# Performance work log

Measured on AMD Instinct MI355X. Metric: run time of the kernel, lower is better.

## Reference

```python
import jax, jax.numpy as jnp
import numpy as np

D_INPUT = 2048
DD_DIM = 512
DD_PAIRS = DD_DIM // 2


def setup_inputs() -> dict:
    key = jax.random.key(0)
    k1, k2, k3 = jax.random.split(key, 3)
    x = jax.random.normal(k1, (4, 4096, D_INPUT), dtype=jnp.float32)
    # Learned projection (zeros at init in torch; use small random for a non-trivial test)
    W = jax.random.normal(k2, (DD_PAIRS, D_INPUT), dtype=jnp.float32) * 0.02
    b = jax.random.normal(k3, (DD_PAIRS,), dtype=jnp.float32) * 0.02
    return {"x": x, "W": W, "b": b}


def reference(x, W, b):
    # x: (B, T, D); W: (P, D); b: (P,) with P = DD_DIM // 2
    deltas = jnp.einsum('btd,pd->btp', x, W) + b          # (B, T, P)
    angles = jnp.cumsum(deltas, axis=1)                   # cumulative phase
    cos, sin = jnp.cos(angles), jnp.sin(angles)
    x1 = x[..., :DD_PAIRS]                                # (B, T, P)
    x2 = x[..., DD_PAIRS:DD_DIM]                          # (B, T, P)
    rotated = jnp.concatenate([x1 * cos - x2 * sin, x2 * cos + x1 * sin], axis=-1)
    return jnp.concatenate([rotated, x[..., DD_DIM:]], axis=-1)
```

## Files before the change

### kernel.cpp

```cpp
#include <hip/hip_runtime.h>
#include <math.h>

#define BB 4
#define TT 4096
#define DDIM 2048
#define PP 256
#define MM (BB*TT)
#define KKDIM 2048
#define CHUNK 32
#define NCHUNK (TT/CHUNK)

#define BK 32
#define KSTEPS (KKDIM/BK)
#define LROW 72

typedef __attribute__((ext_vector_type(8))) short short8;
typedef __attribute__((ext_vector_type(4))) float f32x4;

__device__ __forceinline__ unsigned short f2bf(float f) {
    unsigned u = __float_as_uint(f);
    u += 0x7FFF + ((u >> 16) & 1);
    return (unsigned short)(u >> 16);
}
__device__ __forceinline__ float bf2f(unsigned short h) {
    return __uint_as_float(((unsigned)h) << 16);
}

__device__ __forceinline__ void cvt8(const float4& va, const float4& vb,
                                     short8& hi, short8& lo) {
    float f[8] = {va.x, va.y, va.z, va.w, vb.x, vb.y, vb.z, vb.w};
    #pragma unroll
    for (int j = 0; j < 8; ++j) {
        unsigned short h = f2bf(f[j]);
        hi[j] = (short)h;
        lo[j] = (short)f2bf(f[j] - bf2f(h));
    }
}

__device__ __forceinline__ void cvt4(const float4& v, uint2& hp, uint2& lp) {
    unsigned short h0 = f2bf(v.x), h1 = f2bf(v.y), h2 = f2bf(v.z), h3 = f2bf(v.w);
    unsigned short l0 = f2bf(v.x - bf2f(h0)), l1 = f2bf(v.y - bf2f(h1));
    unsigned short l2 = f2bf(v.z - bf2f(h2)), l3 = f2bf(v.w - bf2f(h3));
    hp.x = (unsigned)h0 | ((unsigned)h1 << 16); hp.y = (unsigned)h2 | ((unsigned)h3 << 16);
    lp.x = (unsigned)l0 | ((unsigned)l1 << 16); lp.y = (unsigned)l2 | ((unsigned)l3 << 16);
}

__global__ __launch_bounds__(256) void prep_wf_k(const float* __restrict__ W,
                                                 unsigned short* __restrict__ Wfh,
                                                 unsigned short* __restrict__ Wfl) {
    const int f = blockIdx.x * 256 + threadIdx.x;
    const int lane = f & 63;
    const int nb   = (f >> 6) & 15;
    const int k0i  = f >> 10;
    const int row  = nb * 16 + (lane & 15);
    const int kk   = k0i * 32 + (lane >> 4) * 8;
    const float* src = W + (size_t)row * KKDIM + kk;
    float4 a = *(const float4*)src;
    float4 b = *(const float4*)(src + 4);
    short8 hi, lo;
    cvt8(a, b, hi, lo);
    *(short8*)(Wfh + (size_t)f * 8) = hi;
    *(short8*)(Wfl + (size_t)f * 8) = lo;
}

#define GBAR()                                                                 \
    do {                                                                       \
        asm volatile("s_waitcnt lgkmcnt(0)" ::: "memory");                     \
        __builtin_amdgcn_sched_barrier(0);                                     \
        __builtin_amdgcn_s_barrier();                                          \
        __builtin_amdgcn_sched_barrier(0);                                     \
    } while (0)

#define GSTEP(CUR, NXT, BHc, BLc, BHn, BLn, ANa0, ANa1, AFa0, AFa1, IT)        \
{                                                                              \
    const int itN_ = (IT) + 1;                                                 \
    const int itF_ = ((IT) + 2 < KSTEPS) ? (IT) + 2 : KSTEPS - 1;              \
                \
    AFa0 = *(const float4*)(xs0 + itF_ * BK);                                  \
    AFa1 = *(const float4*)(xs1 + itF_ * BK);                                  \
                                              \
    const int k0iN_ = (itN_ < KSTEPS) ? itN_ : KSTEPS - 1;                     \
    _Pragma("unroll")                                                          \
    for (int nt = 0; nt < 2; ++nt) {                                           \
        size_t o = bfbase + (size_t)(k0iN_ * 16 + nt) * 512;                   \
        BHn[nt] = *(const short8*)(Wfh + o);                                   \
        BLn[nt] = *(const short8*)(Wfl + o);                                   \
    }                                                                          \
       \
    {                                                                          \
        uint2 hp_, lp_;                                                        \
        cvt4(ANa0, hp_, lp_);                                                  \
        *(uint2*)&Ast[NXT][sidx0]      = hp_;                                  \
        *(uint2*)&Ast[NXT][sidx0 + 32] = lp_;                                  \
        cvt4(ANa1, hp_, lp_);                                                  \
        *(uint2*)&Ast[NXT][sidx1]      = hp_;                                  \
        *(uint2*)&Ast[NXT][sidx1 + 32] = lp_;                                  \
    }                                                                          \
                                    \
    if (docopy && itN_ < KSTEPS) {                                             \
        const int kN_ = itN_ * BK;                                             \
        if (kN_ >= 512) {                                                      \
            *(float4*)(os0 + kN_) = ANa0;                                      \
            *(float4*)(os1 + kN_) = ANa1;                                      \
        }                                                                      \
    }                                                                          \
                                     \
    short8 ah_[2], al_[2];                                                     \
    _Pragma("unroll")                                                          \
    for (int mt = 0; mt < 2; ++mt) {                                           \
        int idx = (wm * 32 + mt * 16 + lm) * LROW + ko * 8;                    \
        ah_[mt] = *(const short8*)&Ast[CUR][idx];                              \
        al_[mt] = *(const short8*)&Ast[CUR][idx + 32];                         \
    }                                                                          \
    _Pragma("unroll")                                                          \
    for (int mt = 0; mt < 2; ++mt)                                             \
        _Pragma("unroll")                                                      \
        for (int nt = 0; nt < 2; ++nt) {                                       \
            f32x4 c = acc[mt][nt];                                             \
            c = __builtin_amdgcn_mfma_f32_16x16x32_bf16(ah_[mt], BHc[nt], c, 0, 0, 0); \
            c = __builtin_amdgcn_mfma_f32_16x16x32_bf16(ah_[mt], BLc[nt], c, 0, 0, 0); \
            c = __builtin_amdgcn_mfma_f32_16x16x32_bf16(al_[mt], BHc[nt], c, 0, 0, 0); \
            acc[mt][nt] = c;                                                   \
        }                                                                      \
    GBAR();                                                                    \
}

__global__ __launch_bounds__(512, 4) void gemm5_k(const float* __restrict__ x,
                                                  const unsigned short* __restrict__ Wfh,
                                                  const unsigned short* __restrict__ Wfl,
                                                  const float* __restrict__ bias,
                                                  float* __restrict__ delta,
                                                  float* __restrict__ csum,
                                                  float* __restrict__ out) {
    __shared__ unsigned short Ast[2][128 * LROW];

    const int hw      = blockIdx.y * 4 + blockIdx.x;
    const int logical = (hw & 7) * 64 + (hw >> 3);
    const int nidx    = logical & 3;
    const int midx    = logical >> 2;
    const int n0      = nidx * 64;
    const int m0      = midx * 128;
    const bool docopy = (nidx == 0);

    const int tid  = threadIdx.x;
    const int w    = tid >> 6;
    const int wm   = w >> 1;
    const int wn   = w & 1;
    const int lane = tid & 63;
    const int lm   = lane & 15;
    const int ko   = lane >> 4;

    const int arow0 = tid >> 3;
    const int ach   = tid & 7;
    const int sidx0 = arow0 * LROW + ach * 4;
    const int sidx1 = (64 + arow0) * LROW + ach * 4;
    const float* xs0 = x + (size_t)(m0 + arow0) * KKDIM + ach * 4;
    const float* xs1 = x + (size_t)(m0 + 64 + arow0) * KKDIM + ach * 4;
    float* os0 = out + (size_t)(m0 + arow0) * DDIM + ach * 4;
    float* os1 = out + (size_t)(m0 + 64 + arow0) * DDIM + ach * 4;

    const size_t bfbase = ((size_t)(nidx * 4 + wn * 2) * 64 + (size_t)lane) * 8;

    f32x4 acc[2][2];
    #pragma unroll
    for (int i = 0; i < 2; ++i)
        #pragma unroll
        for (int j = 0; j < 2; ++j) {
            f32x4 z = {0.f, 0.f, 0.f, 0.f};
            acc[i][j] = z;
        }

    float4 aA0, aA1, aB0, aB1;
    short8 bhA[2], blA[2], bhB[2], blB[2];

    {
        float4 p0 = *(const float4*)(xs0);
        float4 p1 = *(const float4*)(xs1);
        aA0 = *(const float4*)(xs0 + BK);
        aA1 = *(const float4*)(xs1 + BK);
        #pragma unroll
        for (int nt = 0; nt < 2; ++nt) {
            size_t o = bfbase + (size_t)nt * 512;
            bhA[nt] = *(const short8*)(Wfh + o);
            blA[nt] = *(const short8*)(Wfl + o);
        }
        uint2 hp, lp;
        cvt4(p0, hp, lp);
        *(uint2*)&Ast[0][sidx0]      = hp;
        *(uint2*)&Ast[0][sidx0 + 32] = lp;
        cvt4(p1, hp, lp);
        *(uint2*)&Ast[0][sidx1]      = hp;
        *(uint2*)&Ast[0][sidx1 + 32] = lp;
        GBAR();
    }

    for (int it = 0; it < KSTEPS; it += 2) {
        GSTEP(0, 1, bhA, blA, bhB, blB, aA0, aA1, aB0, aB1, it)
        GSTEP(1, 0, bhB, blB, bhA, blA, aB0, aB1, aA0, aA1, it + 1)
    }

    float bsv[2];
    #pragma unroll
    for (int nt = 0; nt < 2; ++nt) bsv[nt] = bias[n0 + wn * 32 + nt * 16 + lm];

    float cs[2] = {0.f, 0.f};
    #pragma unroll
    for (int mt = 0; mt < 2; ++mt)
        #pragma unroll
        for (int nt = 0; nt < 2; ++nt)
            #pragma unroll
            for (int r = 0; r < 4; ++r) {
                float val = acc[mt][nt][r] + bsv[nt];
                int m = m0 + wm * 32 + mt * 16 + ko * 4 + r;
                delta[(size_t)m * PP + n0 + wn * 32 + nt * 16 + lm] = val;
                cs[nt] += val;
            }
    #pragma unroll
    for (int nt = 0; nt < 2; ++nt) {
        float s = cs[nt];
        s += __shfl_xor(s, 16);
        s += __shfl_xor(s, 32);
        if (lane < 16)
            csum[(size_t)(m0 / CHUNK + wm) * PP + n0 + wn * 32 + nt * 16 + lane] = s;
    }
}

__global__ __launch_bounds__(256) void rotate4_k(const float* __restrict__ delta,
                                                 const float* __restrict__ csum,
                                                 const float* __restrict__ x,
                                                 float* __restrict__ out) {
    const int blk = blockIdx.x;
    const int seg = blk & 3;
    const int bc  = blk >> 2;
    const int c   = bc & (NCHUNK - 1);
    const int b   = bc >> 7;
    const int p   = threadIdx.x;

    const float* cs = csum + (size_t)(b * NCHUNK) * PP + p;
    float angle = 0.f;
    int c0 = 0;
    for (; c0 + 16 <= c; c0 += 16) {
        float v[16];
        #pragma unroll
        for (int j = 0; j < 16; ++j) v[j] = cs[(size_t)(c0 + j) * PP];
        #pragma unroll
        for (int j = 0; j < 16; ++j) angle += v[j];
    }
    for (; c0 < c; ++c0) angle += cs[(size_t)c0 * PP];

    const int tbase = bc * CHUNK;
    const float* dp = delta + (size_t)tbase * PP + p;

    const int tpre = seg * 8;
    for (int t = 0; t < tpre; t += 8) {
        float v[8];
        #pragma unroll
        for (int j = 0; j < 8; ++j) v[j] = dp[(size_t)(t + j) * PP];
        #pragma unroll
        for (int j = 0; j < 8; ++j) angle += v[j];
    }

    const float* xp = x + (size_t)tbase * DDIM + p;
    float*       op = out + (size_t)tbase * DDIM + p;
    const float inv2pi = 0.15915494309189535f;

    for (int t0 = tpre; t0 < tpre + 8; t0 += 4) {
        float dv[4], x1v[4], x2v[4];
        #pragma unroll
        for (int j = 0; j < 4; ++j) {
            dv[j]  = dp[(size_t)(t0 + j) * PP];
            x1v[j] = xp[(size_t)(t0 + j) * DDIM];
            x2v[j] = xp[(size_t)(t0 + j) * DDIM + PP];
        }
        #pragma unroll
        for (int j = 0; j < 4; ++j) {
            angle += dv[j];
            float r  = __builtin_amdgcn_fractf(angle * inv2pi);
            float s  = __builtin_amdgcn_sinf(r);
            float co = __builtin_amdgcn_cosf(r);
            op[(size_t)(t0 + j) * DDIM]      = x1v[j] * co - x2v[j] * s;
            op[(size_t)(t0 + j) * DDIM + PP] = x2v[j] * co + x1v[j] * s;
        }
    }
}

__global__ __launch_bounds__(256) void gemm_k(const float* __restrict__ x,
                                              const float* __restrict__ W,
                                              const float* __restrict__ bias,
                                              float* __restrict__ delta,
                                              int dstride, int doff) {
    __shared__ float As[16][68];
    __shared__ float Bs[16][68];
    const int m0  = blockIdx.x * 64;
    const int n0  = blockIdx.y * 64;
    const int tid = threadIdx.x;
    const int lr  = tid >> 2;
    const int lc  = (tid & 3) << 2;
    const int tmi = tid & 15;
    const int tni = tid >> 4;
    float acc[4][4] = {};
    for (int k0 = 0; k0 < KKDIM; k0 += 16) {
        float4 a4 = *(const float4*)(x + (size_t)(m0 + lr) * KKDIM + k0 + lc);
        float4 b4 = *(const float4*)(W + (size_t)(n0 + lr) * KKDIM + k0 + lc);
        __syncthreads();
        As[lc + 0][lr] = a4.x; As[lc + 1][lr] = a4.y;
        As[lc + 2][lr] = a4.z; As[lc + 3][lr] = a4.w;
        Bs[lc + 0][lr] = b4.x; Bs[lc + 1][lr] = b4.y;
        Bs[lc + 2][lr] = b4.z; Bs[lc + 3][lr] = b4.w;
        __syncthreads();
        #pragma unroll
        for (int kk = 0; kk < 16; ++kk) {
            float4 av = *(const float4*)&As[kk][tmi * 4];
            float4 bv = *(const float4*)&Bs[kk][tni * 4];
            float am[4] = {av.x, av.y, av.z, av.w};
            float bn[4] = {bv.x, bv.y, bv.z, bv.w};
            #pragma unroll
            for (int i = 0; i < 4; ++i)
                #pragma unroll
                for (int j = 0; j < 4; ++j)
                    acc[i][j] += am[i] * bn[j];
        }
    }
    const float4 b4 = *(const float4*)(bias + n0 + tni * 4);
    #pragma unroll
    for (int i = 0; i < 4; ++i) {
        size_t m = (size_t)(m0 + tmi * 4 + i);
        float4 o;
        o.x = acc[i][0] + b4.x; o.y = acc[i][1] + b4.y;
        o.z = acc[i][2] + b4.z; o.w = acc[i][3] + b4.w;
        *(float4*)(delta + m * dstride + doff + n0 + tni * 4) = o;
    }
}

__global__ __launch_bounds__(256) void chunksum_k(const float* __restrict__ delta,
                                                  int dstride, int doff,
                                                  float* __restrict__ csum, int cstride) {
    const int bc = blockIdx.x;
    const int b  = bc / NCHUNK;
    const int c  = bc % NCHUNK;
    const int p  = threadIdx.x;
    const int tbase = b * TT + c * CHUNK;
    float s = 0.f;
    #pragma unroll 8
    for (int t = 0; t < CHUNK; ++t)
        s += delta[(size_t)(tbase + t) * dstride + doff + p];
    csum[(size_t)bc * cstride + p] = s;
}

__global__ __launch_bounds__(256) void scan_k(float* __restrict__ csum, int cstride) {
    const int idx = blockIdx.x * 256 + threadIdx.x;
    const int b = idx >> 8;
    const int p = idx & 255;
    float run = 0.f;
    for (int c0 = 0; c0 < NCHUNK; c0 += 8) {
        float v[8];
        #pragma unroll
        for (int j = 0; j < 8; ++j)
            v[j] = csum[(size_t)(b * NCHUNK + c0 + j) * cstride + p];
        #pragma unroll
        for (int j = 0; j < 8; ++j) {
            float t = v[j];
            csum[(size_t)(b * NCHUNK + c0 + j) * cstride + p] = run;
            run += t;
        }
    }
}

__global__ __launch_bounds__(256) void rotate_k(const float* __restrict__ delta,
                                                int dstride, int doff,
                                                const float* __restrict__ csum, int cstride,
                                                const float* __restrict__ x,
                                                float* __restrict__ out) {
    const int bc = blockIdx.x;
    const int p  = threadIdx.x;
    const int tbase = bc * CHUNK;
    float angle = csum[(size_t)bc * cstride + p];
    for (int t = 0; t < CHUNK; ++t) {
        size_t row = (size_t)(tbase + t);
        angle += delta[row * dstride + doff + p];
        float s, co;
        sincosf(angle, &s, &co);
        float x1 = x[row * DDIM + p];
        float x2 = x[row * DDIM + PP + p];
        out[row * DDIM + p]      = x1 * co - x2 * s;
        out[row * DDIM + PP + p] = x2 * co + x1 * s;
    }
}

__global__ __launch_bounds__(256) void copy_k(const float* __restrict__ x,
                                              float* __restrict__ out) {
    const size_t row = (size_t)blockIdx.x * 4 + (threadIdx.x >> 6);
    const int lane = threadIdx.x & 63;
    const int col = 512 + (blockIdx.y * 64 + lane) * 4;
    const size_t a = row * DDIM + col;
    *(float4*)(out + a) = *(const float4*)(x + a);
}

extern "C" void kernel_launch(void* const* d_in, const int* in_sizes, int n_in,
                              void* d_out, int out_size, void* d_ws, size_t ws_size,
                              hipStream_t stream) {
    const float* x    = (const float*)d_in[0];
    const float* W    = (const float*)d_in[1];
    const float* bias = (const float*)d_in[2];
    float* out = (float*)d_out;

    const size_t delta_elems = (size_t)MM * PP;
    const size_t csum_elems  = (size_t)BB * NCHUNK * PP;
    const size_t w_elems     = (size_t)PP * KKDIM;
    const size_t need = (delta_elems + csum_elems) * sizeof(float)
                      + 2 * w_elems * sizeof(unsigned short);

    if (ws_size >= need) {
        float* delta = (float*)d_ws;
        float* csum  = (float*)d_ws + delta_elems;
        unsigned short* Wfh = (unsigned short*)(csum + csum_elems);
        unsigned short* Wfl = Wfh + w_elems;
        prep_wf_k<<<256, 256, 0, stream>>>(W, Wfh, Wfl);
        gemm5_k<<<dim3(4, MM / 128), 512, 0, stream>>>(x, Wfh, Wfl, bias,
                                                       delta, csum, out);
        rotate4_k<<<BB * NCHUNK * 4, 256, 0, stream>>>(delta, csum, x, out);
    } else {
        float* delta = out; const int dstride = DDIM, doff = 512;
        float* csum  = out + 768; const int cstride = DDIM;
        gemm_k<<<dim3(MM / 64, PP / 64), 256, 0, stream>>>(x, W, bias, delta, dstride, doff);
        chunksum_k<<<BB * NCHUNK, 256, 0, stream>>>(delta, dstride, doff, csum, cstride);
        scan_k<<<(BB * PP) / 256, 256, 0, stream>>>(csum, cstride);
        rotate_k<<<BB * NCHUNK, 256, 0, stream>>>(delta, dstride, doff, csum, cstride, x, out);
        copy_k<<<dim3(MM / 4, 6), 256, 0, stream>>>(x, out);
    }
}
```

Baseline: 325.5 us.

## Restructure GEMM so each wave stages its own A rows and drop block barriers

The GEMM kernel moves from 512 threads with a 4x2 wave grid and a shared A tile to 256 threads where each wave owns 32 rows and stages its own private, XOR-swizzled LDS slice. Because no wave reads another wave's data, the per-k-step block barrier is removed. Each wave now covers a 32x64 tile (twice the N width), doubling B register fragments per step. The aim is to cut barrier stalls and LDS bank conflicts. In exchange, each wave loads the full B tile itself, so global and L2 traffic for W doubles, register pressure rises, and launch bounds drop to 2 blocks per CU.

Result: slower. 352.2 us (+8.2%).

```diff
diff --git a/kernel.cpp b/kernel.cpp
--- a/kernel.cpp
+++ b/kernel.cpp
@@ -12,7 +12,7 @@
 
 #define BK 32
 #define KSTEPS (KKDIM/BK)
-#define LROW 72
+#define LSLICE (32*128)
 
 typedef __attribute__((ext_vector_type(8))) short short8;
 typedef __attribute__((ext_vector_type(4))) float f32x4;
@@ -43,6 +43,10 @@
     unsigned short l2 = f2bf(v.z - bf2f(h2)), l3 = f2bf(v.w - bf2f(h3));
     hp.x = (unsigned)h0 | ((unsigned)h1 << 16); hp.y = (unsigned)h2 | ((unsigned)h3 << 16);
     lp.x = (unsigned)l0 | ((unsigned)l1 << 16); lp.y = (unsigned)l2 | ((unsigned)l3 << 16);
+}
+
+__device__ __forceinline__ int aoff(int row, int inner) {
+    return row * 128 + (inner ^ ((row & 7) << 4));
 }
 
 __global__ __launch_bounds__(256) void prep_wf_k(const float* __restrict__ W,
@@ -63,76 +67,68 @@
     *(short8*)(Wfl + (size_t)f * 8) = lo;
 }
 
-#define GBAR()                                                                 \
-    do {                                                                       \
-        asm volatile("s_waitcnt lgkmcnt(0)" ::: "memory");                     \
-        __builtin_amdgcn_sched_barrier(0);                                     \
-        __builtin_amdgcn_s_barrier();                                          \
-        __builtin_amdgcn_sched_barrier(0);                                     \
-    } while (0)
-
-#define GSTEP(CUR, NXT, BHc, BLc, BHn, BLn, ANa0, ANa1, AFa0, AFa1, IT)        \
+__device__ __forceinline__ void stageA(const float4 a[4], unsigned char* sb,
+                                       int r_, int q_) {
+    uint2 hp[4], lp[4];
+    #pragma unroll
+    for (int j = 0; j < 4; ++j) cvt4(a[j], hp[j], lp[j]);
+    uint4 h01 = {hp[0].x, hp[0].y, hp[1].x, hp[1].y};
+    uint4 h23 = {hp[2].x, hp[2].y, hp[3].x, hp[3].y};
+    uint4 l01 = {lp[0].x, lp[0].y, lp[1].x, lp[1].y};
+    uint4 l23 = {lp[2].x, lp[2].y, lp[3].x, lp[3].y};
+    *(uint4*)(sb + aoff(r_, q_ * 32))           = h01;
+    *(uint4*)(sb + aoff(r_, q_ * 32 + 16))      = h23;
+    *(uint4*)(sb + aoff(r_, 64 + q_ * 32))      = l01;
+    *(uint4*)(sb + aoff(r_, 64 + q_ * 32 + 16)) = l23;
+}
+
+#define GSTEP6(CUR, NXT, AC, AP, BC, BN, IT)                                   \
 {                                                                              \
-    const int itN_ = (IT) + 1;                                                 \
-    const int itF_ = ((IT) + 2 < KSTEPS) ? (IT) + 2 : KSTEPS - 1;              \
-                \
-    AFa0 = *(const float4*)(xs0 + itF_ * BK);                                  \
-    AFa1 = *(const float4*)(xs1 + itF_ * BK);                                  \
-                                              \
-    const int k0iN_ = (itN_ < KSTEPS) ? itN_ : KSTEPS - 1;                     \
+    const int itA_ = ((IT) + 2 < KSTEPS) ? (IT) + 2 : KSTEPS - 1;              \
+    const int itB_ = ((IT) + 1 < KSTEPS) ? (IT) + 1 : KSTEPS - 1;              \
     _Pragma("unroll")                                                          \
-    for (int nt = 0; nt < 2; ++nt) {                                           \
-        size_t o = bfbase + (size_t)(k0iN_ * 16 + nt) * 512;                   \
-        BHn[nt] = *(const short8*)(Wfh + o);                                   \
-        BLn[nt] = *(const short8*)(Wfl + o);                                   \
+    for (int j = 0; j < 4; ++j)                                                \
+        AP[j] = *(const float4*)(xsrc + (size_t)itA_ * BK + j * 4);            \
+    _Pragma("unroll")                                                          \
+    for (int nt = 0; nt < 4; ++nt) {                                           \
+        size_t o = bfbase + (size_t)itB_ * 8192 + (size_t)nt * 512;            \
+        BN[2 * nt]     = *(const short8*)(Wfh + o);                            \
+        BN[2 * nt + 1] = *(const short8*)(Wfl + o);                            \
     }                                                                          \
-       \
-    {                                                                          \
-        uint2 hp_, lp_;                                                        \
-        cvt4(ANa0, hp_, lp_);                                                  \
-        *(uint2*)&Ast[NXT][sidx0]      = hp_;                                  \
-        *(uint2*)&Ast[NXT][sidx0 + 32] = lp_;                                  \
-        cvt4(ANa1, hp_, lp_);                                                  \
-        *(uint2*)&Ast[NXT][sidx1]      = hp_;                                  \
-        *(uint2*)&Ast[NXT][sidx1 + 32] = lp_;                                  \
+    stageA(AC, sbW + (NXT) * LSLICE, r_, q_);         \
+    if (docopy && (IT) + 1 < KSTEPS && ((IT) + 1) * BK >= 512) {               \
+        _Pragma("unroll")                                                      \
+        for (int j = 0; j < 4; ++j)                                            \
+            *(float4*)(osrc + (size_t)((IT) + 1) * BK + j * 4) = AC[j];        \
     }                                                                          \
-                                    \
-    if (docopy && itN_ < KSTEPS) {                                             \
-        const int kN_ = itN_ * BK;                                             \
-        if (kN_ >= 512) {                                                      \
-            *(float4*)(os0 + kN_) = ANa0;                                      \
-            *(float4*)(os1 + kN_) = ANa1;                                      \
-        }                                                                      \
-    }                                                                          \
-                                     \
     short8 ah_[2], al_[2];                                                     \
     _Pragma("unroll")                                                          \
     for (int mt = 0; mt < 2; ++mt) {                                           \
-        int idx = (wm * 32 + mt * 16 + lm) * LROW + ko * 8;                    \
-        ah_[mt] = *(const short8*)&Ast[CUR][idx];                              \
-        al_[mt] = *(const short8*)&Ast[CUR][idx + 32];                         \
+        const unsigned char* sr = sbW + (CUR) * LSLICE;                        \
+        int row = mt * 16 + lm;                                                \
+        ah_[mt] = *(const short8*)(sr + aoff(row, ko * 16));                   \
+        al_[mt] = *(const short8*)(sr + aoff(row, 64 + ko * 16));              \
     }                                                                          \
     _Pragma("unroll")                                                          \
     for (int mt = 0; mt < 2; ++mt)                                             \
         _Pragma("unroll")                                                      \
-        for (int nt = 0; nt < 2; ++nt) {                                       \
+        for (int nt = 0; nt < 4; ++nt) {                                       \
             f32x4 c = acc[mt][nt];                                             \
-            c = __builtin_amdgcn_mfma_f32_16x16x32_bf16(ah_[mt], BHc[nt], c, 0, 0, 0); \
-            c = __builtin_amdgcn_mfma_f32_16x16x32_bf16(ah_[mt], BLc[nt], c, 0, 0, 0); \
-            c = __builtin_amdgcn_mfma_f32_16x16x32_bf16(al_[mt], BHc[nt], c, 0, 0, 0); \
+            c = __builtin_amdgcn_mfma_f32_16x16x32_bf16(ah_[mt], BC[2*nt],   c, 0, 0, 0); \
+            c = __builtin_amdgcn_mfma_f32_16x16x32_bf16(ah_[mt], BC[2*nt+1], c, 0, 0, 0); \
+            c = __builtin_amdgcn_mfma_f32_16x16x32_bf16(al_[mt], BC[2*nt],   c, 0, 0, 0); \
             acc[mt][nt] = c;                                                   \
         }                                                                      \
-    GBAR();                                                                    \
-}
-
-__global__ __launch_bounds__(512, 4) void gemm5_k(const float* __restrict__ x,
+}
+
+__global__ __launch_bounds__(256, 2) void gemm6_k(const float* __restrict__ x,
                                                   const unsigned short* __restrict__ Wfh,
                                                   const unsigned short* __restrict__ Wfl,
                                                   const float* __restrict__ bias,
                                                   float* __restrict__ delta,
                                                   float* __restrict__ csum,
                                                   float* __restrict__ out) {
-    __shared__ unsigned short Ast[2][128 * LROW];
+    __shared__ unsigned char Asb[4][2][LSLICE];
 
     const int hw      = blockIdx.y * 4 + blockIdx.x;
     const int logical = (hw & 7) * 64 + (hw >> 3);
@@ -144,84 +140,73 @@
 
     const int tid  = threadIdx.x;
     const int w    = tid >> 6;
-    const int wm   = w >> 1;
-    const int wn   = w & 1;
     const int lane = tid & 63;
     const int lm   = lane & 15;
     const int ko   = lane >> 4;
-
-    const int arow0 = tid >> 3;
-    const int ach   = tid & 7;
-    const int sidx0 = arow0 * LROW + ach * 4;
-    const int sidx1 = (64 + arow0) * LROW + ach * 4;
-    const float* xs0 = x + (size_t)(m0 + arow0) * KKDIM + ach * 4;
-    const float* xs1 = x + (size_t)(m0 + 64 + arow0) * KKDIM + ach * 4;
-    float* os0 = out + (size_t)(m0 + arow0) * DDIM + ach * 4;
-    float* os1 = out + (size_t)(m0 + 64 + arow0) * DDIM + ach * 4;
-
-    const size_t bfbase = ((size_t)(nidx * 4 + wn * 2) * 64 + (size_t)lane) * 8;
-
-    f32x4 acc[2][2];
+    const int r_   = lane >> 1;
+    const int q_   = lane & 1;
+
+    unsigned char* sbW = &Asb[w][0][0];
+    const float* xsrc = x + (size_t)(m0 + w * 32 + r_) * KKDIM + q_ * 16;
+    float*       osrc = out + (size_t)(m0 + w * 32 + r_) * DDIM + q_ * 16;
+
+    const size_t bfbase = ((size_t)(nidx * 4) * 64 + (size_t)lane) * 8;
+
+    f32x4 acc[2][4];
     #pragma unroll
     for (int i = 0; i < 2; ++i)
         #pragma unroll
-        for (int j = 0; j < 2; ++j) {
+        for (int j = 0; j < 4; ++j) {
             f32x4 z = {0.f, 0.f, 0.f, 0.f};
             acc[i][j] = z;
         }
 
-    float4 aA0, aA1, aB0, aB1;
-    short8 bhA[2], blA[2], bhB[2], blB[2];
+    float4 aA[4], aB[4];
+    short8 bA[8], bB[8];
 
     {
-        float4 p0 = *(const float4*)(xs0);
-        float4 p1 = *(const float4*)(xs1);
-        aA0 = *(const float4*)(xs0 + BK);
-        aA1 = *(const float4*)(xs1 + BK);
-        #pragma unroll
-        for (int nt = 0; nt < 2; ++nt) {
+        float4 t0[4];
+        #pragma unroll
+        for (int j = 0; j < 4; ++j) t0[j] = *(const float4*)(xsrc + j * 4);
+        #pragma unroll
+        for (int j = 0; j < 4; ++j) aA[j] = *(const float4*)(xsrc + BK + j * 4);
+        #pragma unroll
+        for (int nt = 0; nt < 4; ++nt) {
             size_t o = bfbase + (size_t)nt * 512;
-            bhA[nt] = *(const short8*)(Wfh + o);
-            blA[nt] = *(const short8*)(Wfl + o);
-        }
-        uint2 hp, lp;
-        cvt4(p0, hp, lp);
-        *(uint2*)&Ast[0][sidx0]      = hp;
-        *(uint2*)&Ast[0][sidx0 + 32] = lp;
-        cvt4(p1, hp, lp);
-        *(uint2*)&Ast[0][sidx1]      = hp;
-        *(uint2*)&Ast[0][sidx1 + 32] = lp;
-        GBAR();
+            bA[2 * nt]     = *(const short8*)(Wfh + o);
+            bA[2 * nt + 1] = *(const short8*)(Wfl + o);
+        }
+        stageA(t0, sbW, r_, q_);
     }
 
     for (int it = 0; it < KSTEPS; it += 2) {
-        GSTEP(0, 1, bhA, blA, bhB, blB, aA0, aA1, aB0, aB1, it)
-        GSTEP(1, 0, bhB, blB, bhA, blA, aB0, aB1, aA0, aA1, it + 1)
-    }
-
-    float bsv[2];
-    #pragma unroll
-    for (int nt = 0; nt < 2; ++nt) bsv[nt] = bias[n0 + wn * 32 + nt * 16 + lm];
-
-    float cs[2] = {0.f, 0.f};
+        GSTEP6(0, 1, aA, aB, bA, bB, it)
+        GSTEP6(1, 0, aB, aA, bB, bA, it + 1)
+    }
+
+    float bsv[4];
+    #pragma unroll
+    for (int nt = 0; nt < 4; ++nt) bsv[nt] = bias[n0 + nt * 16 + lm];
+
+    float cs[4] = {0.f, 0.f, 0.f, 0.f};
     #pragma unroll
     for (int mt = 0; mt < 2; ++mt)
         #pragma unroll
-        for (int nt = 0; nt < 2; ++nt)
+        for (int nt = 0; nt < 4; ++nt)
             #pragma unroll
             for (int r = 0; r < 4; ++r) {
                 float val = acc[mt][nt][r] + bsv[nt];
-                int m = m0 + wm * 32 + mt * 16 + ko * 4 + r;
-                delta[(size_t)m * PP + n0 + wn * 32 + nt * 16 + lm] = val;
+                int m = m0 + w * 32 + mt * 16 + ko * 4 + r;
+                delta[(size_t)m * PP + n0 + nt * 16 + lm] = val;
                 cs[nt] += val;
             }
     #pragma unroll
-    for (int nt = 0; nt < 2; ++nt) {
+    for (int nt = 0; nt < 4; ++nt) {
         float s = cs[nt];
         s += __shfl_xor(s, 16);
         s += __shfl_xor(s, 32);
         if (lane < 16)
-            csum[(size_t)(m0 / CHUNK + wm) * PP + n0 + wn * 32 + nt * 16 + lane] = s;
+            csum[(size_t)(m0 / CHUNK + w) * PP + n0 + nt * 16 + lane] = s;
     }
 }
 
@@ -416,7 +401,7 @@
         unsigned short* Wfh = (unsigned short*)(csum + csum_elems);
         unsigned short* Wfl = Wfh + w_elems;
         prep_wf_k<<<256, 256, 0, stream>>>(W, Wfh, Wfl);
-        gemm5_k<<<dim3(4, MM / 128), 512, 0, stream>>>(x, Wfh, Wfl, bias,
+        gemm6_k<<<dim3(4, MM / 128), 256, 0, stream>>>(x, Wfh, Wfl, bias,
                                                        delta, csum, out);
         rotate4_k<<<BB * NCHUNK * 4, 256, 0, stream>>>(delta, csum, x, out);
     } else {
```
